# Kernel tuning notes

Hardware: AMD Instinct MI355X
Metric: run time of the kernel (lower is better)

Reference implementation:

```python
import jax, jax.numpy as jnp
import numpy as np

N = 20000
F_IN = 128
HID = 128
HEADS = 8
NCLS = 18
NEG_SLOPE = 0.2


def setup_inputs() -> dict:
    key = jax.random.key(0)
    ks = jax.random.split(key, 12)
    x = jax.random.normal(ks[0], (N, F_IN), dtype=jnp.float32)
    edge_index = jax.random.randint(ks[1], (2, 200000), 0, N)
    sc1 = 1.0 / np.sqrt(F_IN)
    sc2 = 1.0 / np.sqrt(HEADS * HID)
    W1 = jax.random.normal(ks[2], (F_IN, HEADS * HID), dtype=jnp.float32) * sc1
    a1_src = jax.random.normal(ks[3], (HEADS, HID), dtype=jnp.float32) * sc1
    a1_dst = jax.random.normal(ks[4], (HEADS, HID), dtype=jnp.float32) * sc1
    b1 = jnp.zeros((HEADS * HID,), dtype=jnp.float32)
    W2 = jax.random.normal(ks[5], (HEADS * HID, NCLS), dtype=jnp.float32) * sc2
    a2_src = jax.random.normal(ks[6], (1, NCLS), dtype=jnp.float32) * sc2
    a2_dst = jax.random.normal(ks[7], (1, NCLS), dtype=jnp.float32) * sc2
    b2 = jnp.zeros((NCLS,), dtype=jnp.float32)
    return {"x": x, "edge_index": edge_index, "W1": W1, "a1_src": a1_src,
            "a1_dst": a1_dst, "b1": b1, "W2": W2, "a2_src": a2_src,
            "a2_dst": a2_dst, "b2": b2}


def gat_conv(x, src, dst, W, a_src, a_dst, b, heads, out_ch):
    n = x.shape[0]
    h = (x @ W).reshape(n, heads, out_ch)              # [N,H,C]
    alpha_s = jnp.sum(h * a_src, axis=-1)              # [N,H]
    alpha_d = jnp.sum(h * a_dst, axis=-1)              # [N,H]
    e = jax.nn.leaky_relu(alpha_s[src] + alpha_d[dst], NEG_SLOPE)  # [E,H]
    # per-destination softmax (segment softmax)
    m = jax.ops.segment_max(e, dst, num_segments=n)
    e = jnp.exp(e - m[dst])
    z = jax.ops.segment_sum(e, dst, num_segments=n)
    alpha = e / (z[dst] + 1e-16)                       # [E,H]
    out = jax.ops.segment_sum(alpha[:, :, None] * h[src], dst, num_segments=n)
    return out.reshape(n, heads * out_ch) + b


def reference(x, edge_index, W1, a1_src, a1_dst, b1, W2, a2_src, a2_dst, b2):
    n = x.shape[0]
    # PyG GATConv adds self-loops by default
    loops = jnp.arange(n, dtype=edge_index.dtype)
    src = jnp.concatenate([edge_index[0], loops])
    dst = jnp.concatenate([edge_index[1], loops])
    h = gat_conv(x, src, dst, W1, a1_src, a1_dst, b1, HEADS, HID)
    h = jax.nn.relu(h)
    # F.dropout(training=self.training) is identity in eval mode
    out = gat_conv(h, src, dst, W2, a2_src, a2_dst, b2, 1, NCLS)
    return out
```

## Files before the change

### kernel.cpp

```cpp
#include <hip/hip_runtime.h>
#include <math.h>

#define FIN 128
#define NH 8
#define HC 128
#define HD (NH*HC)
#define NC 18
#define NCP 24
#define NEG 0.2f

typedef __attribute__((ext_vector_type(8))) short bf16x8;
typedef __attribute__((ext_vector_type(4))) float f32x4;

__device__ __forceinline__ float lrelu(float v){ return v > 0.f ? v : NEG*v; }

__device__ __forceinline__ unsigned short f2b(float f){
  unsigned u = __float_as_uint(f);
  unsigned r = (u + 0x7fffu + ((u >> 16) & 1u)) >> 16;
  return (unsigned short)r;
}
__device__ __forceinline__ float b2f_lo(unsigned u){ return __uint_as_float(u << 16); }
__device__ __forceinline__ float b2f_hi(unsigned u){ return __uint_as_float(u & 0xffff0000u); }

__device__ __forceinline__ void acc8(float* a, float w, uint4 r){
  a[0] += w*b2f_lo(r.x); a[1] += w*b2f_hi(r.x);
  a[2] += w*b2f_lo(r.y); a[3] += w*b2f_hi(r.y);
  a[4] += w*b2f_lo(r.z); a[5] += w*b2f_hi(r.z);
  a[6] += w*b2f_lo(r.w); a[7] += w*b2f_hi(r.w);
}

__global__ void hist_k(const int* __restrict__ ei, int E0, int N, int* __restrict__ deg){
  int e = blockIdx.x*256 + threadIdx.x;
  int tot = E0 + N;
  if (e >= tot) return;
  int dst = (e < E0) ? ei[E0 + e] : (e - E0);
  atomicAdd(&deg[dst], 1);
}

__global__ __launch_bounds__(1024) void scan_k(const int* __restrict__ deg, int N,
                                               int* __restrict__ off, int* __restrict__ cursor){
  __shared__ int wsum[16];
  __shared__ int s_carry;
  int t = threadIdx.x, lane = t & 63, wid = t >> 6;
  if (t == 0) s_carry = 0;
  __syncthreads();
  for (int base = 0; base < N; base += 1024) {
    int i = base + t;
    int v = (i < N) ? deg[i] : 0;
    int x = v;
    #pragma unroll
    for (int o = 1; o < 64; o <<= 1) {
      int y = __shfl_up(x, o, 64);
      if (lane >= o) x += y;
    }
    if (lane == 63) wsum[wid] = x;
    __syncthreads();
    if (wid == 0) {
      int wv = (lane < 16) ? wsum[lane] : 0;
      #pragma unroll
      for (int o = 1; o < 16; o <<= 1) {
        int y = __shfl_up(wv, o, 64);
        if (lane >= o) wv += y;
      }
      if (lane < 16) wsum[lane] = wv;
    }
    __syncthreads();
    int woff = (wid > 0) ? wsum[wid-1] : 0;
    int carry = s_carry;
    int exc = x - v + woff + carry;
    if (i < N) { off[i] = exc; cursor[i] = exc; }
    __syncthreads();
    if (t == 1023) s_carry = carry + wsum[15];
    __syncthreads();
  }
  if (t == 0) off[N] = s_carry;
}

__global__ void scatter_k(const int* __restrict__ ei, int E0, int N,
                          int* __restrict__ cursor, int* __restrict__ csr){
  int e = blockIdx.x*256 + threadIdx.x;
  int tot = E0 + N;
  if (e >= tot) return;
  int src, dst;
  if (e < E0) { src = ei[e]; dst = ei[E0 + e]; }
  else        { src = e - E0; dst = src; }
  int p = atomicAdd(&cursor[dst], 1);
  csr[p] = src;
}

__global__ __launch_bounds__(256) void xcvt_k(const float* __restrict__ x,
                                              unsigned short* __restrict__ xb, int total8){
  int i = blockIdx.x*256 + threadIdx.x;
  if (i >= total8) return;
  const float4* p = (const float4*)x + (size_t)i*2;
  float4 a = p[0], b = p[1];
  uint4 o;
  o.x = (unsigned)f2b(a.x) | ((unsigned)f2b(a.y) << 16);
  o.y = (unsigned)f2b(a.z) | ((unsigned)f2b(a.w) << 16);
  o.z = (unsigned)f2b(b.x) | ((unsigned)f2b(b.y) << 16);
  o.w = (unsigned)f2b(b.z) | ((unsigned)f2b(b.w) << 16);
  ((uint4*)xb)[i] = o;
}

__global__ __launch_bounds__(256) void w1t_k(const float* __restrict__ W1,
                                             unsigned short* __restrict__ w1t){
  __shared__ unsigned short sT[FIN][64+2];
  int t = threadIdx.x;
  int n0 = blockIdx.x * 64;
  #pragma unroll
  for (int i = 0; i < 32; ++i) {
    int idx = i*256 + t;
    int k = idx >> 6, nl = idx & 63;
    sT[k][nl] = f2b(W1[(size_t)k*HD + n0 + nl]);
  }
  __syncthreads();
  #pragma unroll
  for (int i = 0; i < 16; ++i) {
    int nl = i*4 + (t >> 6);
    int kp = t & 63;
    unsigned u = (unsigned)sT[2*kp][nl] | ((unsigned)sT[2*kp+1][nl] << 16);
    *(unsigned*)&w1t[(size_t)(n0+nl)*FIN + 2*kp] = u;
  }
}

__global__ __launch_bounds__(256) void w2cvt_k(const float* __restrict__ W2,
                                               unsigned short* __restrict__ w2b){
  int idx = blockIdx.x*256 + threadIdx.x;
  if (idx >= HD*NC) return;
  int k = idx / NC, c = idx - k*NC;
  w2b[k*NCP + c] = f2b(W2[idx]);
}

__global__ __launch_bounds__(256) void gemm1_mfma_k(const unsigned short* __restrict__ xb,
                                                    const unsigned short* __restrict__ w1t,
                                                    unsigned short* __restrict__ g1b, int N){
  __shared__ unsigned short sA[128][136];
  __shared__ unsigned short sB[128][136];
  int t = threadIdx.x, lane = t & 63, wid = t >> 6;
  int bm = blockIdx.x * 128;
  int bn = blockIdx.y * 128;
  #pragma unroll
  for (int i = 0; i < 2; ++i) {
    int idx = i*256 + t;
    int row = idx >> 2, seg = idx & 3;
    int gm = bm + row;
    uint4 a0,a1,a2,a3;
    if (gm < N) {
      const uint4* gp = (const uint4*)(xb + (size_t)gm*FIN + seg*32);
      a0 = gp[0]; a1 = gp[1]; a2 = gp[2]; a3 = gp[3];
    } else {
      a0 = a1 = a2 = a3 = make_uint4(0,0,0,0);
    }
    uint4* lp = (uint4*)&sA[row][seg*32];
    lp[0]=a0; lp[1]=a1; lp[2]=a2; lp[3]=a3;
  }
  #pragma unroll
  for (int i = 0; i < 2; ++i) {
    int idx = i*256 + t;
    int row = idx >> 2, seg = idx & 3;
    const uint4* gp = (const uint4*)(w1t + (size_t)(bn + row)*FIN + seg*32);
    uint4* lp = (uint4*)&sB[row][seg*32];
    lp[0]=gp[0]; lp[1]=gp[1]; lp[2]=gp[2]; lp[3]=gp[3];
  }
  __syncthreads();
  int wr = wid >> 1, wc = wid & 1;
  int lr = lane & 15, kb = lane >> 4;
  f32x4 acc[4][4];
  #pragma unroll
  for (int mi = 0; mi < 4; ++mi)
    #pragma unroll
    for (int ni = 0; ni < 4; ++ni) {
      f32x4 z = {0.f, 0.f, 0.f, 0.f};
      acc[mi][ni] = z;
    }
  #pragma unroll
  for (int ks = 0; ks < 4; ++ks) {
    int ko = ks*32 + kb*8;
    bf16x8 a[4], b[4];
    #pragma unroll
    for (int mi = 0; mi < 4; ++mi)
      a[mi] = *(const bf16x8*)&sA[wr*64 + mi*16 + lr][ko];
    #pragma unroll
    for (int ni = 0; ni < 4; ++ni)
      b[ni] = *(const bf16x8*)&sB[wc*64 + ni*16 + lr][ko];
    #pragma unroll
    for (int mi = 0; mi < 4; ++mi)
      #pragma unroll
      for (int ni = 0; ni < 4; ++ni)
        acc[mi][ni] = __builtin_amdgcn_mfma_f32_16x16x32_bf16(a[mi], b[ni], acc[mi][ni], 0, 0, 0);
  }
  #pragma unroll
  for (int mi = 0; mi < 4; ++mi)
    #pragma unroll
    for (int ni = 0; ni < 4; ++ni) {
      int col = bn + wc*64 + ni*16 + lr;
      #pragma unroll
      for (int r = 0; r < 4; ++r) {
        int row = bm + wr*64 + mi*16 + kb*4 + r;
        if (row < N) g1b[(size_t)row*HD + col] = f2b(acc[mi][ni][r]);
      }
    }
}

__global__ __launch_bounds__(256) void alpha1_k(const unsigned short* __restrict__ g1b,
    const float* __restrict__ a1s, const float* __restrict__ a1d,
    float* __restrict__ as1, float* __restrict__ ad1, int N){
  int t = threadIdx.x, lane = t & 63, wid = t >> 6;
  int n = blockIdx.x*4 + wid;
  if (n >= N) return;
  int c0 = lane * 16;
  int h = lane >> 3;
  const uint4* p = (const uint4*)(g1b + (size_t)n*HD) + lane*2;
  uint4 r0 = p[0], r1 = p[1];
  float hv[16];
  hv[0]=b2f_lo(r0.x); hv[1]=b2f_hi(r0.x); hv[2]=b2f_lo(r0.y); hv[3]=b2f_hi(r0.y);
  hv[4]=b2f_lo(r0.z); hv[5]=b2f_hi(r0.z); hv[6]=b2f_lo(r0.w); hv[7]=b2f_hi(r0.w);
  hv[8]=b2f_lo(r1.x); hv[9]=b2f_hi(r1.x); hv[10]=b2f_lo(r1.y); hv[11]=b2f_hi(r1.y);
  hv[12]=b2f_lo(r1.z); hv[13]=b2f_hi(r1.z); hv[14]=b2f_lo(r1.w); hv[15]=b2f_hi(r1.w);
  float s = 0.f, dd = 0.f;
  #pragma unroll
  for (int q = 0; q < 4; ++q) {
    float4 av = *(const float4*)&a1s[c0 + q*4];
    float4 bv = *(const float4*)&a1d[c0 + q*4];
    s  += hv[q*4+0]*av.x + hv[q*4+1]*av.y + hv[q*4+2]*av.z + hv[q*4+3]*av.w;
    dd += hv[q*4+0]*bv.x + hv[q*4+1]*bv.y + hv[q*4+2]*bv.z + hv[q*4+3]*bv.w;
  }
  #pragma unroll
  for (int o = 1; o < 8; o <<= 1) {
    s  += __shfl_xor(s, o, 8);
    dd += __shfl_xor(dd, o, 8);
  }
  if ((lane & 7) == 0) { as1[n*NH + h] = s; ad1[n*NH + h] = dd; }
}

__global__ __launch_bounds__(256) void attn1_k(const unsigned short* __restrict__ g1b,
    const float* __restrict__ as1, const float* __restrict__ ad1,
    const int* __restrict__ off, const int* __restrict__ csr,
    const float* __restrict__ b1, unsigned short* __restrict__ hb, int N){
  int t = threadIdx.x, lane = t & 63, wid = t >> 6;
  int d = blockIdx.x*4 + wid;
  if (d >= N) return;
  int beg = off[d], deg = off[d+1] - beg;
  int hg = lane >> 3;
  float adg = ad1[d*NH + hg];
  float m = -1e30f, z = 0.f;
  float acc[16];
  #pragma unroll
  for (int i = 0; i < 16; ++i) acc[i] = 0.f;

  int j = 0;
  for (; j + 4 <= deg; j += 4) {
    int s0 = csr[beg+j+0], s1 = csr[beg+j+1], s2 = csr[beg+j+2], s3 = csr[beg+j+3];
    const uint4* p0 = (const uint4*)(g1b + (size_t)s0*HD) + lane*2;
    const uint4* p1 = (const uint4*)(g1b + (size_t)s1*HD) + lane*2;
    const uint4* p2 = (const uint4*)(g1b + (size_t)s2*HD) + lane*2;
    const uint4* p3 = (const uint4*)(g1b + (size_t)s3*HD) + lane*2;
    uint4 r00 = p0[0], r01 = p0[1];
    uint4 r10 = p1[0], r11 = p1[1];
    uint4 r20 = p2[0], r21 = p2[1];
    uint4 r30 = p3[0], r31 = p3[1];
    float e0 = lrelu(as1[s0*NH+hg] + adg);
    float e1 = lrelu(as1[s1*NH+hg] + adg);
    float e2 = lrelu(as1[s2*NH+hg] + adg);
    float e3 = lrelu(as1[s3*NH+hg] + adg);
    float em = fmaxf(fmaxf(e0,e1), fmaxf(e2,e3));
    if (em > m) {
      float sc = __expf(m - em);
      z *= sc;
      #pragma unroll
      for (int i = 0; i < 16; ++i) acc[i] *= sc;
      m = em;
    }
    float w0 = __expf(e0 - m), w1 = __expf(e1 - m);
    float w2 = __expf(e2 - m), w3 = __expf(e3 - m);
    z += w0 + w1 + w2 + w3;
    acc8(acc, w0, r00); acc8(acc+8, w0, r01);
    acc8(acc, w1, r10); acc8(acc+8, w1, r11);
    acc8(acc, w2, r20); acc8(acc+8, w2, r21);
    acc8(acc, w3, r30); acc8(acc+8, w3, r31);
  }
  for (; j < deg; ++j) {
    int s = csr[beg+j];
    const uint4* p = (const uint4*)(g1b + (size_t)s*HD) + lane*2;
    uint4 r0 = p[0], r1 = p[1];
    float e = lrelu(as1[s*NH+hg] + adg);
    if (e > m) {
      float sc = __expf(m - e);
      z *= sc;
      #pragma unroll
      for (int i = 0; i < 16; ++i) acc[i] *= sc;
      m = e;
    }
    float w = __expf(e - m);
    z += w;
    acc8(acc, w, r0); acc8(acc+8, w, r1);
  }

  float zinv = 1.f / (z + 1e-16f);
  int cb = lane*16;
  uint o[8];
  #pragma unroll
  for (int q = 0; q < 4; ++q) {
    float4 bv = *(const float4*)&b1[cb + q*4];
    float v0 = fmaxf(acc[q*4+0]*zinv + bv.x, 0.f);
    float v1 = fmaxf(acc[q*4+1]*zinv + bv.y, 0.f);
    float v2 = fmaxf(acc[q*4+2]*zinv + bv.z, 0.f);
    float v3 = fmaxf(acc[q*4+3]*zinv + bv.w, 0.f);
    o[q*2+0] = (unsigned)f2b(v0) | ((unsigned)f2b(v1) << 16);
    o[q*2+1] = (unsigned)f2b(v2) | ((unsigned)f2b(v3) << 16);
  }
  uint4* dst = (uint4*)(hb + (size_t)d*HD) + lane*2;
  dst[0] = make_uint4(o[0], o[1], o[2], o[3]);
  dst[1] = make_uint4(o[4], o[5], o[6], o[7]);
}

__global__ __launch_bounds__(256) void gemm2_k(const unsigned short* __restrict__ hb,
    const unsigned short* __restrict__ w2b, const float* __restrict__ a2s_g, const float* __restrict__ a2d_g,
    float* __restrict__ g2, float* __restrict__ as2, float* __restrict__ ad2, int N){
  __shared__ float red[3][64][NC+1];
  int t = threadIdx.x, lane = t & 63, wid = t >> 6;
  int n0 = blockIdx.x * 64;
  int n = n0 + lane;
  bool valid = (n < N);
  float acc[NC];
  #pragma unroll
  for (int c = 0; c < NC; ++c) acc[c] = 0.f;
  int k0beg = wid * 256;
  for (int k0 = k0beg; k0 < k0beg + 256; k0 += 8) {
    uint4 raw = valid ? *(const uint4*)(hb + (size_t)n*HD + k0) : make_uint4(0,0,0,0);
    float a[8];
    a[0]=b2f_lo(raw.x); a[1]=b2f_hi(raw.x); a[2]=b2f_lo(raw.y); a[3]=b2f_hi(raw.y);
    a[4]=b2f_lo(raw.z); a[5]=b2f_hi(raw.z); a[6]=b2f_lo(raw.w); a[7]=b2f_hi(raw.w);
    #pragma unroll
    for (int kk = 0; kk < 8; ++kk) {
      const unsigned* wr = (const unsigned*)(w2b + (size_t)(k0 + kk)*NCP);
      uint4 u0 = *(const uint4*)(wr);
      uint4 u1 = *(const uint4*)(wr + 4);
      unsigned u2 = wr[8];
      float av = a[kk];
      acc[0]  += av * b2f_lo(u0.x); acc[1]  += av * b2f_hi(u0.x);
      acc[2]  += av * b2f_lo(u0.y); acc[3]  += av * b2f_hi(u0.y);
      acc[4]  += av * b2f_lo(u0.z); acc[5]  += av * b2f_hi(u0.z);
      acc[6]  += av * b2f_lo(u0.w); acc[7]  += av * b2f_hi(u0.w);
      acc[8]  += av * b2f_lo(u1.x); acc[9]  += av * b2f_hi(u1.x);
      acc[10] += av * b2f_lo(u1.y); acc[11] += av * b2f_hi(u1.y);
      acc[12] += av * b2f_lo(u1.z); acc[13] += av * b2f_hi(u1.z);
      acc[14] += av * b2f_lo(u1.w); acc[15] += av * b2f_hi(u1.w);
      acc[16] += av * b2f_lo(u2);   acc[17] += av * b2f_hi(u2);
    }
  }
  if (wid > 0) {
    #pragma unroll
    for (int c = 0; c < NC; ++c) red[wid-1][lane][c] = acc[c];
  }
  __syncthreads();
  if (wid == 0 && valid) {
    float tot[NC];
    #pragma unroll
    for (int c = 0; c < NC; ++c)
      tot[c] = acc[c] + red[0][lane][c] + red[1][lane][c] + red[2][lane][c];
    float s = 0.f, dd = 0.f;
    #pragma unroll
    for (int c = 0; c < NC; ++c) {
      s  += tot[c]*a2s_g[c];
      dd += tot[c]*a2d_g[c];
      g2[(size_t)n*NC + c] = tot[c];
    }
    as2[n] = s; ad2[n] = dd;
  }
}

__global__ __launch_bounds__(256) void attn2_k(const float* __restrict__ g2,
    const float* __restrict__ as2, const float* __restrict__ ad2,
    const int* __restrict__ off, const int* __restrict__ csr,
    const float* __restrict__ b2, float* __restrict__ out, int N){
  int t = threadIdx.x, lane = t & 63, wid = t >> 6;
  int d = blockIdx.x*4 + wid;
  if (d >= N) return;
  int beg = off[d], deg = off[d+1] - beg;
  float adv = ad2[d];
  int g = lane / 18;
  int c = lane - g*18;
  float m = -1e30f, z = 0.f, acc = 0.f;
  if (g < 3) {
    int j = g;
    for (; j + 3 < deg; j += 6) {
      int sa = csr[beg+j], sb = csr[beg+j+3];
      float va = g2[(size_t)sa*NC + c];
      float vb = g2[(size_t)sb*NC + c];
      float ea = lrelu(as2[sa] + adv);
      float eb = lrelu(as2[sb] + adv);
      float em = fmaxf(ea, eb);
      if (em > m) { float sc = __expf(m - em); z *= sc; acc *= sc; m = em; }
      float wa = __expf(ea - m), wb = __expf(eb - m);
      z += wa + wb;
      acc += wa*va + wb*vb;
    }
    for (; j < deg; j += 3) {
      int s = csr[beg+j];
      float v = g2[(size_t)s*NC + c];
      float e = lrelu(as2[s] + adv);
      if (e > m) { float sc = __expf(m - e); z *= sc; acc *= sc; m = e; }
      float w = __expf(e - m);
      z += w;
      acc += w*v;
    }
  }
  float m0 = __shfl(m, 0),  m1 = __shfl(m, 18), m2 = __shfl(m, 36);
  float M  = fmaxf(m0, fmaxf(m1, m2));
  float e0 = __expf(m0 - M), e1 = __expf(m1 - M), e2 = __expf(m2 - M);
  float z0 = __shfl(z, 0),  z1 = __shfl(z, 18), z2 = __shfl(z, 36);
  int cl = (lane < NC) ? lane : 0;
  float a0 = __shfl(acc, cl), a1 = __shfl(acc, cl+18), a2 = __shfl(acc, cl+36);
  if (lane < NC) {
    float Z = z0*e0 + z1*e1 + z2*e2;
    float A = a0*e0 + a1*e1 + a2*e2;
    out[(size_t)d*NC + lane] = A / (Z + 1e-16f) + b2[lane];
  }
}

extern "C" void kernel_launch(void* const* d_in, const int* in_sizes, int n_in,
                              void* d_out, int out_size, void* d_ws, size_t ws_size,
                              hipStream_t stream){
  const float* x   = (const float*)d_in[0];
  const int*   ei  = (const int*)d_in[1];
  const float* W1  = (const float*)d_in[2];
  const float* a1s = (const float*)d_in[3];
  const float* a1d = (const float*)d_in[4];
  const float* b1  = (const float*)d_in[5];
  const float* W2  = (const float*)d_in[6];
  const float* a2s = (const float*)d_in[7];
  const float* a2d = (const float*)d_in[8];
  const float* b2  = (const float*)d_in[9];
  float* out = (float*)d_out;
  int N  = in_sizes[0] / FIN;
  int E0 = in_sizes[1] / 2;
  int Etot = E0 + N;

  float* as1 = (float*)d_ws;
  float* ad1 = as1 + (size_t)N*NH;
  float* g2  = ad1 + (size_t)N*NH;
  float* as2 = g2 + (size_t)N*NC;
  float* ad2 = as2 + N;
  unsigned short* g1b = (unsigned short*)(ad2 + N);
  unsigned short* hb  = g1b + (size_t)N*HD;
  int* deg    = (int*)(hb + (size_t)N*HD);
  int* off    = deg + N;
  int* cursor = off + N + 4;
  int* csr    = cursor + N;
  unsigned short* w2b = (unsigned short*)(csr + Etot);
  unsigned short* xb  = hb;
  unsigned short* w1t = hb + (size_t)N*FIN;

  hipMemsetAsync(deg, 0, sizeof(int)*(size_t)N, stream);
  hist_k<<<(Etot+255)/256, 256, 0, stream>>>(ei, E0, N, deg);
  scan_k<<<1, 1024, 0, stream>>>(deg, N, off, cursor);
  scatter_k<<<(Etot+255)/256, 256, 0, stream>>>(ei, E0, N, cursor, csr);

  int total8 = N*FIN/8;
  xcvt_k<<<(total8+255)/256, 256, 0, stream>>>(x, xb, total8);
  w1t_k<<<HD/64, 256, 0, stream>>>(W1, w1t);
  w2cvt_k<<<(HD*NC+255)/256, 256, 0, stream>>>(W2, w2b);

  dim3 g1grid((N+127)/128, HD/128);
  gemm1_mfma_k<<<g1grid, 256, 0, stream>>>(xb, w1t, g1b, N);
  alpha1_k<<<(N+3)/4, 256, 0, stream>>>(g1b, a1s, a1d, as1, ad1, N);
  attn1_k<<<(N+3)/4, 256, 0, stream>>>(g1b, as1, ad1, off, csr, b1, hb, N);
  gemm2_k<<<(N+63)/64, 256, 0, stream>>>(hb, w2b, a2s, a2d, g2, as2, ad2, N);
  attn2_k<<<(N+3)/4, 256, 0, stream>>>(g2, as2, ad2, off, csr, b2, out, N);
}
```

Measured before the change: 293.4 us.

## Fuse prep kernels into one launch and fold alpha1 into GEMM1 epilogue

The x conversion, W1 transpose, W2 conversion and degree histogram now run as one kernel launch, with blocks dispatched by index range. The attention logits for layer 1 are computed in the GEMM1 epilogue from fp32 accumulators, using shuffle reductions and an LDS merge across the two column waves, which removes the separate alpha1 kernel and its re-read of g1b. The GEMM1 output is also staged through LDS so each row is written to global memory as contiguous 16-byte vectors instead of scattered 2-byte stores. Costs are extra shuffles and syncs in the GEMM epilogue, and logits now come from fp32 rather than bf16-rounded values.

```diff
diff --git a/kernel.cpp b/kernel.cpp
--- a/kernel.cpp
+++ b/kernel.cpp
@@ -27,14 +27,6 @@
   a[2] += w*b2f_lo(r.y); a[3] += w*b2f_hi(r.y);
   a[4] += w*b2f_lo(r.z); a[5] += w*b2f_hi(r.z);
   a[6] += w*b2f_lo(r.w); a[7] += w*b2f_hi(r.w);
-}
-
-__global__ void hist_k(const int* __restrict__ ei, int E0, int N, int* __restrict__ deg){
-  int e = blockIdx.x*256 + threadIdx.x;
-  int tot = E0 + N;
-  if (e >= tot) return;
-  int dst = (e < E0) ? ei[E0 + e] : (e - E0);
-  atomicAdd(&deg[dst], 1);
 }
 
 __global__ __launch_bounds__(1024) void scan_k(const int* __restrict__ deg, int N,
@@ -88,57 +80,78 @@
   csr[p] = src;
 }
 
-__global__ __launch_bounds__(256) void xcvt_k(const float* __restrict__ x,
-                                              unsigned short* __restrict__ xb, int total8){
-  int i = blockIdx.x*256 + threadIdx.x;
-  if (i >= total8) return;
-  const float4* p = (const float4*)x + (size_t)i*2;
-  float4 a = p[0], b = p[1];
-  uint4 o;
-  o.x = (unsigned)f2b(a.x) | ((unsigned)f2b(a.y) << 16);
-  o.y = (unsigned)f2b(a.z) | ((unsigned)f2b(a.w) << 16);
-  o.z = (unsigned)f2b(b.x) | ((unsigned)f2b(b.y) << 16);
-  o.w = (unsigned)f2b(b.z) | ((unsigned)f2b(b.w) << 16);
-  ((uint4*)xb)[i] = o;
-}
-
-__global__ __launch_bounds__(256) void w1t_k(const float* __restrict__ W1,
-                                             unsigned short* __restrict__ w1t){
+__global__ __launch_bounds__(256) void prep_k(const float* __restrict__ x,
+    const float* __restrict__ W1, const float* __restrict__ W2,
+    const int* __restrict__ ei,
+    unsigned short* __restrict__ xb, unsigned short* __restrict__ w1t,
+    unsigned short* __restrict__ w2b, int* __restrict__ deg,
+    int total8, int bX, int E0, int N, int bH){
   __shared__ unsigned short sT[FIN][64+2];
-  int t = threadIdx.x;
-  int n0 = blockIdx.x * 64;
-  #pragma unroll
-  for (int i = 0; i < 32; ++i) {
-    int idx = i*256 + t;
-    int k = idx >> 6, nl = idx & 63;
-    sT[k][nl] = f2b(W1[(size_t)k*HD + n0 + nl]);
-  }
-  __syncthreads();
-  #pragma unroll
-  for (int i = 0; i < 16; ++i) {
-    int nl = i*4 + (t >> 6);
-    int kp = t & 63;
-    unsigned u = (unsigned)sT[2*kp][nl] | ((unsigned)sT[2*kp+1][nl] << 16);
-    *(unsigned*)&w1t[(size_t)(n0+nl)*FIN + 2*kp] = u;
-  }
-}
-
-__global__ __launch_bounds__(256) void w2cvt_k(const float* __restrict__ W2,
-                                               unsigned short* __restrict__ w2b){
-  int idx = blockIdx.x*256 + threadIdx.x;
-  if (idx >= HD*NC) return;
-  int k = idx / NC, c = idx - k*NC;
-  w2b[k*NCP + c] = f2b(W2[idx]);
+  int b = blockIdx.x, t = threadIdx.x;
+  if (b < bX) {
+    int i = b*256 + t;
+    if (i < total8) {
+      const float4* p = (const float4*)x + (size_t)i*2;
+      float4 a = p[0], c = p[1];
+      uint4 o;
+      o.x = (unsigned)f2b(a.x) | ((unsigned)f2b(a.y) << 16);
+      o.y = (unsigned)f2b(a.z) | ((unsigned)f2b(a.w) << 16);
+      o.z = (unsigned)f2b(c.x) | ((unsigned)f2b(c.y) << 16);
+      o.w = (unsigned)f2b(c.z) | ((unsigned)f2b(c.w) << 16);
+      ((uint4*)xb)[i] = o;
+    }
+    return;
+  }
+  b -= bX;
+  if (b < 16) {
+    int n0 = b * 64;
+    #pragma unroll
+    for (int i = 0; i < 32; ++i) {
+      int idx = i*256 + t;
+      int k = idx >> 6, nl = idx & 63;
+      sT[k][nl] = f2b(W1[(size_t)k*HD + n0 + nl]);
+    }
+    __syncthreads();
+    #pragma unroll
+    for (int i = 0; i < 16; ++i) {
+      int nl = i*4 + (t >> 6);
+      int kp = t & 63;
+      unsigned u = (unsigned)sT[2*kp][nl] | ((unsigned)sT[2*kp+1][nl] << 16);
+      *(unsigned*)&w1t[(size_t)(n0+nl)*FIN + 2*kp] = u;
+    }
+    return;
+  }
+  b -= 16;
+  if (b < 72) {
+    int idx = b*256 + t;
+    if (idx < HD*NC) {
+      int k = idx / NC, c = idx - k*NC;
+      w2b[k*NCP + c] = f2b(W2[idx]);
+    }
+    return;
+  }
+  b -= 72;
+  {
+    int e = b*256 + t;
+    int tot = E0 + N;
+    if (e >= tot) return;
+    int dst = (e < E0) ? ei[E0 + e] : (e - E0);
+    atomicAdd(&deg[dst], 1);
+  }
 }
 
 __global__ __launch_bounds__(256) void gemm1_mfma_k(const unsigned short* __restrict__ xb,
-                                                    const unsigned short* __restrict__ w1t,
-                                                    unsigned short* __restrict__ g1b, int N){
+    const unsigned short* __restrict__ w1t,
+    const float* __restrict__ a1s, const float* __restrict__ a1d,
+    unsigned short* __restrict__ g1b, float* __restrict__ as1, float* __restrict__ ad1,
+    int N){
   __shared__ unsigned short sA[128][136];
   __shared__ unsigned short sB[128][136];
+  __shared__ float sAs[2][128], sAd[2][128];
   int t = threadIdx.x, lane = t & 63, wid = t >> 6;
   int bm = blockIdx.x * 128;
-  int bn = blockIdx.y * 128;
+  int head = blockIdx.y;
+  int bn = head * 128;
   #pragma unroll
   for (int i = 0; i < 2; ++i) {
     int idx = i*256 + t;
@@ -189,48 +202,59 @@
       for (int ni = 0; ni < 4; ++ni)
         acc[mi][ni] = __builtin_amdgcn_mfma_f32_16x16x32_bf16(a[mi], b[ni], acc[mi][ni], 0, 0, 0);
   }
+  __syncthreads();
+
+  float a1sv[4], a1dv[4];
+  #pragma unroll
+  for (int ni = 0; ni < 4; ++ni) {
+    int c = wc*64 + ni*16 + lr;
+    a1sv[ni] = a1s[head*HC + c];
+    a1dv[ni] = a1d[head*HC + c];
+  }
+  #pragma unroll
+  for (int mi = 0; mi < 4; ++mi) {
+    #pragma unroll
+    for (int r = 0; r < 4; ++r) {
+      float ps = acc[mi][0][r]*a1sv[0] + acc[mi][1][r]*a1sv[1]
+               + acc[mi][2][r]*a1sv[2] + acc[mi][3][r]*a1sv[3];
+      float pd = acc[mi][0][r]*a1dv[0] + acc[mi][1][r]*a1dv[1]
+               + acc[mi][2][r]*a1dv[2] + acc[mi][3][r]*a1dv[3];
+      #pragma unroll
+      for (int o = 1; o < 16; o <<= 1) {
+        ps += __shfl_xor(ps, o, 64);
+        pd += __shfl_xor(pd, o, 64);
+      }
+      if (lr == 0) {
+        int row = wr*64 + mi*16 + kb*4 + r;
+        sAs[wc][row] = ps;
+        sAd[wc][row] = pd;
+      }
+    }
+  }
   #pragma unroll
   for (int mi = 0; mi < 4; ++mi)
     #pragma unroll
     for (int ni = 0; ni < 4; ++ni) {
-      int col = bn + wc*64 + ni*16 + lr;
-      #pragma unroll
-      for (int r = 0; r < 4; ++r) {
-        int row = bm + wr*64 + mi*16 + kb*4 + r;
-        if (row < N) g1b[(size_t)row*HD + col] = f2b(acc[mi][ni][r]);
-      }
-    }
-}
-
-__global__ __launch_bounds__(256) void alpha1_k(const unsigned short* __restrict__ g1b,
-    const float* __restrict__ a1s, const float* __restrict__ a1d,
-    float* __restrict__ as1, float* __restrict__ ad1, int N){
-  int t = threadIdx.x, lane = t & 63, wid = t >> 6;
-  int n = blockIdx.x*4 + wid;
-  if (n >= N) return;
-  int c0 = lane * 16;
-  int h = lane >> 3;
-  const uint4* p = (const uint4*)(g1b + (size_t)n*HD) + lane*2;
-  uint4 r0 = p[0], r1 = p[1];
-  float hv[16];
-  hv[0]=b2f_lo(r0.x); hv[1]=b2f_hi(r0.x); hv[2]=b2f_lo(r0.y); hv[3]=b2f_hi(r0.y);
-  hv[4]=b2f_lo(r0.z); hv[5]=b2f_hi(r0.z); hv[6]=b2f_lo(r0.w); hv[7]=b2f_hi(r0.w);
-  hv[8]=b2f_lo(r1.x); hv[9]=b2f_hi(r1.x); hv[10]=b2f_lo(r1.y); hv[11]=b2f_hi(r1.y);
-  hv[12]=b2f_lo(r1.z); hv[13]=b2f_hi(r1.z); hv[14]=b2f_lo(r1.w); hv[15]=b2f_hi(r1.w);
-  float s = 0.f, dd = 0.f;
-  #pragma unroll
-  for (int q = 0; q < 4; ++q) {
-    float4 av = *(const float4*)&a1s[c0 + q*4];
-    float4 bv = *(const float4*)&a1d[c0 + q*4];
-    s  += hv[q*4+0]*av.x + hv[q*4+1]*av.y + hv[q*4+2]*av.z + hv[q*4+3]*av.w;
-    dd += hv[q*4+0]*bv.x + hv[q*4+1]*bv.y + hv[q*4+2]*bv.z + hv[q*4+3]*bv.w;
-  }
-  #pragma unroll
-  for (int o = 1; o < 8; o <<= 1) {
-    s  += __shfl_xor(s, o, 8);
-    dd += __shfl_xor(dd, o, 8);
-  }
-  if ((lane & 7) == 0) { as1[n*NH + h] = s; ad1[n*NH + h] = dd; }
+      int col = wc*64 + ni*16 + lr;
+      #pragma unroll
+      for (int r = 0; r < 4; ++r)
+        sA[wr*64 + mi*16 + kb*4 + r][col] = f2b(acc[mi][ni][r]);
+    }
+  __syncthreads();
+  {
+    int row = t >> 1, half = t & 1;
+    int grow = bm + row;
+    if (grow < N) {
+      uint4* dst = (uint4*)(g1b + (size_t)grow*HD + bn + half*64);
+      const uint4* src = (const uint4*)&sA[row][half*64];
+      #pragma unroll
+      for (int q = 0; q < 8; ++q) dst[q] = src[q];
+    }
+    if (t < 128 && bm + t < N) {
+      as1[(size_t)(bm + t)*NH + head] = sAs[0][t] + sAs[1][t];
+      ad1[(size_t)(bm + t)*NH + head] = sAd[0][t] + sAd[1][t];
+    }
+  }
 }
 
 __global__ __launch_bounds__(256) void attn1_k(const unsigned short* __restrict__ g1b,
@@ -453,18 +477,17 @@
   unsigned short* w1t = hb + (size_t)N*FIN;
 
   hipMemsetAsync(deg, 0, sizeof(int)*(size_t)N, stream);
-  hist_k<<<(Etot+255)/256, 256, 0, stream>>>(ei, E0, N, deg);
+
+  int total8 = N*FIN/8;
+  int bX = (total8 + 255)/256;
+  int bH = (Etot + 255)/256;
+  prep_k<<<bX + 16 + 72 + bH, 256, 0, stream>>>(x, W1, W2, ei, xb, w1t, w2b, deg,
+                                                total8, bX, E0, N, bH);
   scan_k<<<1, 1024, 0, stream>>>(deg, N, off, cursor);
   scatter_k<<<(Etot+255)/256, 256, 0, stream>>>(ei, E0, N, cursor, csr);
 
-  int total8 = N*FIN/8;
-  xcvt_k<<<(total8+255)/256, 256, 0, stream>>>(x, xb, total8);
-  w1t_k<<<HD/64, 256, 0, stream>>>(W1, w1t);
-  w2cvt_k<<<(HD*NC+255)/256, 256, 0, stream>>>(W2, w2b);
-
   dim3 g1grid((N+127)/128, HD/128);
-  gemm1_mfma_k<<<g1grid, 256, 0, stream>>>(xb, w1t, g1b, N);
-  alpha1_k<<<(N+3)/4, 256, 0, stream>>>(g1b, a1s, a1d, as1, ad1, N);
+  gemm1_mfma_k<<<g1grid, 256, 0, stream>>>(xb, w1t, a1s, a1d, g1b, as1, ad1, N);
   attn1_k<<<(N+3)/4, 256, 0, stream>>>(g1b, as1, ad1, off, csr, b1, hb, N);
   gemm2_k<<<(N+63)/64, 256, 0, stream>>>(hb, w2b, a2s, a2d, g2, as2, ad2, N);
   attn2_k<<<(N+3)/4, 256, 0, stream>>>(g2, as2, ad2, off, csr, b2, out, N);
```

Measured after the change: 293.2 us. No clear change (-0.1%).
